# Performance work log

Measured on AMD Instinct MI355X. Metric: run time of the kernel, lower is better.

The kernel has to match this reference:

```python
import jax, jax.numpy as jnp
import numpy as np

B, C, H, L = 4, 1, 1024, 8192
KD, NS = 64, 4  # kernel_dim, num_scales


def _interp_linear(x, out_len):
    """F.interpolate(mode='linear', align_corners=False) along last axis."""
    in_len = x.shape[-1]
    if out_len == in_len:
        return x
    scale = out_len / in_len
    coord = (jnp.arange(out_len, dtype=jnp.float32) + 0.5) / scale - 0.5
    coord = jnp.clip(coord, 0.0, in_len - 1)
    lo = jnp.floor(coord).astype(jnp.int32)
    hi = jnp.minimum(lo + 1, in_len - 1)
    w = coord - lo.astype(jnp.float32)
    return x[..., lo] * (1.0 - w) + x[..., hi] * w


def setup_inputs() -> dict:
    key = jax.random.key(0)
    ks = jax.random.split(key, 8)
    u = jax.random.normal(ks[0], (B, H, L), jnp.float32)
    k0 = jax.random.normal(ks[1], (C, H, KD), jnp.float32)
    k1 = jax.random.normal(ks[2], (C, H, KD), jnp.float32)
    k2 = jax.random.normal(ks[3], (C, H, KD), jnp.float32)
    k3 = jax.random.normal(ks[4], (C, H, KD), jnp.float32)
    D = jax.random.normal(ks[5], (C, H), jnp.float32)
    W = jax.random.normal(ks[6], (H, C * H), jnp.float32) / np.float32(np.sqrt(C * H))
    b = jnp.zeros((H,), jnp.float32)
    return {"u": u, "k0": k0, "k1": k1, "k2": k2, "k3": k3, "D": D, "W": W, "b": b}


def reference(u, k0, k1, k2, k3, D, W, b):
    Lq = u.shape[-1]
    kernels = [k0, k1, k2, k3]
    total = KD * 2 ** (NS - 1)  # 512
    # multi-scale kernel build: interpolate -> right-pad -> scale -> sum
    parts = []
    for i in range(NS):
        ki = _interp_linear(kernels[i], KD * 2 ** i)
        ki = jnp.pad(ki, ((0, 0), (0, 0), (0, total - KD * 2 ** i)))
        parts.append(ki * (2.0 ** (NS - i - 1)))
    k = parts[0] + parts[1] + parts[2] + parts[3]  # (C,H,512)
    # fit to sequence length L
    if k.shape[-1] > Lq:
        k = k[..., :Lq]
    elif k.shape[-1] < Lq:
        k = jnp.pad(k, ((0, 0), (0, 0), (0, Lq - k.shape[-1])))
    # detached kernel norm
    knorm = jax.lax.stop_gradient(
        jnp.linalg.norm(k, axis=-1, keepdims=True))
    k = k / knorm
    # FFT long convolution
    n = 2 * Lq
    k_f = jnp.fft.rfft(k, n=n)              # (C,H,L+1) complex
    u_f = jnp.fft.rfft(u, n=n)              # (B,H,L+1) complex
    y_f = jnp.einsum('bhl,chl->bchl', u_f, k_f)
    y = jnp.fft.irfft(y_f, n=n)[..., :Lq]   # (B,C,H,L)
    # D skip (outer product)
    y = y + jnp.einsum('bhl,ch->bchl', u, D)
    y = y.reshape(y.shape[0], C * H, Lq)    # (B,C*H,L)
    # activation (exact gelu, torch default), dropout=Identity, norm=Identity
    y = jax.nn.gelu(y, approximate=False)
    # output_linear: 1x1 conv (C*H -> H) with bias, Identity post-activation
    y = jnp.einsum('bfl,of->bol', y, W) + b[None, :, None]
    return y
```

## Files before the change

kernel.cpp:

```cpp
#include <hip/hip_runtime.h>
#include <cstdint>
#include <cstddef>

#define HH 1024
#define LL 8192
#define NB 4
#define KD 64
#define KLEN 512

typedef float v4f  __attribute__((ext_vector_type(4)));
typedef float v16f __attribute__((ext_vector_type(16)));
typedef short v8s  __attribute__((ext_vector_type(8)));

__device__ __forceinline__ unsigned short f2bf(float f) {
  union { float f; unsigned int u; } x; x.f = f;
  unsigned int r = x.u + 0x7fffu + ((x.u >> 16) & 1u);
  return (unsigned short)(r >> 16);
}

__global__ __launch_bounds__(512) void build_k_kernel(
    const float* __restrict__ k0, const float* __restrict__ k1,
    const float* __restrict__ k2, const float* __restrict__ k3,
    float* __restrict__ kout) {
  __shared__ float lk[4][KD];
  __shared__ float red[512];
  const int h = blockIdx.x;
  const int t = threadIdx.x;
  if (t < 256) {
    int i = t >> 6, j = t & 63;
    const float* src = (i == 0) ? k0 : (i == 1) ? k1 : (i == 2) ? k2 : k3;
    lk[i][j] = src[h * KD + j];
  }
  __syncthreads();
  float kt = 0.f;
#pragma unroll
  for (int i = 0; i < 4; i++) {
    int len = KD << i;
    if (t < len) {
      float inv = 1.0f / (float)(1 << i);
      float c = ((float)t + 0.5f) * inv - 0.5f;
      c = fminf(fmaxf(c, 0.0f), 63.0f);
      int lo = (int)floorf(c);
      int hi = min(lo + 1, 63);
      float w = c - (float)lo;
      float v = lk[i][lo] * (1.0f - w) + lk[i][hi] * w;
      kt += v * (float)(1 << (3 - i));
    }
  }
  red[t] = kt * kt;
  __syncthreads();
  for (int s = 256; s > 0; s >>= 1) {
    if (t < s) red[t] += red[t + s];
    __syncthreads();
  }
  float norm = sqrtf(red[0]);
  kout[h * KLEN + t] = kt / norm;
}

__global__ void w2bf_kernel(const float* __restrict__ W,
                            unsigned short* __restrict__ Wb, int n) {
  int i = blockIdx.x * blockDim.x + threadIdx.x;
  if (i < n) Wb[i] = f2bf(W[i]);
}

__global__ __launch_bounds__(256) void conv_kernel(
    const float* __restrict__ u, const float* __restrict__ kk,
    const float* __restrict__ D, unsigned short* __restrict__ g) {
  __shared__ __align__(16) unsigned short Apk[34 * 512];
  __shared__ __align__(16) unsigned short su[512 + LL];
  __shared__ __align__(16) float skk[KLEN];

  const int h = blockIdx.x;
  const int tid = threadIdx.x;
  const int w = tid >> 6;
  const int ln = tid & 63;
  const int n = ln & 31;
  const int q = ln >> 5;

  if (tid < 128) *(float4*)(skk + tid * 4) = *(const float4*)(kk + (size_t)h * KLEN + tid * 4);
  __syncthreads();

#pragma unroll 4
  for (int e = 0; e < 68; ++e) {
    int idx = e * 256 + tid;
    int s = idx >> 9;
    int lane = (idx >> 3) & 63;
    int j = idx & 7;
    int m = lane & 31, q2 = lane >> 5;
    int c = ((s & 1) << 4) + (q2 << 3) + j;
    int t = ((s >> 1) << 5) + m - c;
    Apk[idx] = (t >= 0 && t < KLEN) ? f2bf(skk[t]) : (unsigned short)0;
  }

  const float Dh = D[h];
  const int b_base0 = 512 + 32 * (w * 64 + n) + 8 * q;
  const int b_base1 = b_base0 + 1024;

  for (int b = 0; b < NB; ++b) {
    __syncthreads();
    const float* __restrict__ urow = u + ((size_t)b * HH + h) * LL;
    if (tid < 64) {
      uint4 z; z.x = 0; z.y = 0; z.z = 0; z.w = 0;
      *(uint4*)(su + tid * 8) = z;
    }
#pragma unroll
    for (int r = 0; r < 8; ++r) {
      int i = r * 1024 + tid * 4;
      float4 v = *(const float4*)(urow + i);
      uint2 p;
      p.x = (unsigned)f2bf(v.x) | ((unsigned)f2bf(v.y) << 16);
      p.y = (unsigned)f2bf(v.z) | ((unsigned)f2bf(v.w) << 16);
      *(uint2*)(su + 512 + i) = p;
    }
    __syncthreads();

    v16f acc0, acc1;
#pragma unroll
    for (int r = 0; r < 16; ++r) { acc0[r] = 0.f; acc1[r] = 0.f; }

#pragma unroll
    for (int s = 0; s < 34; ++s) {
      const int off = ((s & 1) << 4) - ((s >> 1) << 5);
      v8s af = *(const v8s*)(Apk + (s << 9) + (ln << 3));
      v8s b0 = *(const v8s*)(su + b_base0 + off);
      v8s b1 = *(const v8s*)(su + b_base1 + off);
      acc0 = __builtin_amdgcn_mfma_f32_32x32x16_bf16(af, b0, acc0, 0, 0, 0);
      acc1 = __builtin_amdgcn_mfma_f32_32x32x16_bf16(af, b1, acc1, 0, 0, 0);
    }

    unsigned short* grow = g + ((size_t)b * HH + h) * LL;
#pragma unroll
    for (int t = 0; t < 2; ++t) {
      const int i0 = w * 64 + t * 32;
#pragma unroll
      for (int rg = 0; rg < 4; ++rg) {
        const int l = 32 * (i0 + n) + 8 * rg + 4 * q;
        float4 uu = *(const float4*)(urow + l);
        const float* up = (const float*)&uu;
        unsigned short hb[4];
#pragma unroll
        for (int rr = 0; rr < 4; ++rr) {
          float y = (t ? acc1[rg * 4 + rr] : acc0[rg * 4 + rr]) + Dh * up[rr];
          float ge = 0.5f * y * (1.0f + erff(y * 0.70710678118654752f));
          hb[rr] = f2bf(ge);
        }
        uint2 p;
        p.x = (unsigned)hb[0] | ((unsigned)hb[1] << 16);
        p.y = (unsigned)hb[2] | ((unsigned)hb[3] << 16);
        *(uint2*)(grow + l) = p;
      }
    }
  }
}

__global__ __launch_bounds__(256) void transpose_kernel(
    const unsigned short* __restrict__ g, unsigned short* __restrict__ gt) {
  __shared__ unsigned short s[64][65];
  const int bid = blockIdx.x;
  const int lc = bid & 127;
  const int hc = (bid >> 7) & 15;
  const int b = bid >> 11;
  const int l0 = lc * 64, h0 = hc * 64;
  const int tid = threadIdx.x;
  const int seg = tid & 7, rr = tid >> 3;
#pragma unroll
  for (int p = 0; p < 2; p++) {
    int r = p * 32 + rr;
    uint4 v = *(const uint4*)(g + (size_t)(b * HH + h0 + r) * LL + l0 + seg * 8);
    s[r][seg * 8 + 0] = (unsigned short)(v.x);
    s[r][seg * 8 + 1] = (unsigned short)(v.x >> 16);
    s[r][seg * 8 + 2] = (unsigned short)(v.y);
    s[r][seg * 8 + 3] = (unsigned short)(v.y >> 16);
    s[r][seg * 8 + 4] = (unsigned short)(v.z);
    s[r][seg * 8 + 5] = (unsigned short)(v.z >> 16);
    s[r][seg * 8 + 6] = (unsigned short)(v.w);
    s[r][seg * 8 + 7] = (unsigned short)(v.w >> 16);
  }
  __syncthreads();
#pragma unroll
  for (int p = 0; p < 2; p++) {
    int lr = p * 32 + rr;
    unsigned int a0 = (unsigned)s[seg * 8 + 0][lr] | ((unsigned)s[seg * 8 + 1][lr] << 16);
    unsigned int a1 = (unsigned)s[seg * 8 + 2][lr] | ((unsigned)s[seg * 8 + 3][lr] << 16);
    unsigned int a2 = (unsigned)s[seg * 8 + 4][lr] | ((unsigned)s[seg * 8 + 5][lr] << 16);
    unsigned int a3 = (unsigned)s[seg * 8 + 6][lr] | ((unsigned)s[seg * 8 + 7][lr] << 16);
    uint4 ov; ov.x = a0; ov.y = a1; ov.z = a2; ov.w = a3;
    *(uint4*)(gt + (size_t)(b * LL + l0 + lr) * HH + h0 + seg * 8) = ov;
  }
}

__device__ __forceinline__ void gll16(const void* g, void* l) {
  __builtin_amdgcn_global_load_lds(
      (const __attribute__((address_space(1))) unsigned int*)g,
      (__attribute__((address_space(3))) unsigned int*)l, 16, 0, 0);
}

__global__ __launch_bounds__(256) void gemm_kernel(
    const unsigned short* __restrict__ A,
    const unsigned short* __restrict__ Bt,
    const float* __restrict__ bias, float* __restrict__ out) {
  __shared__ __align__(16) unsigned short sA[128 * 32];
  __shared__ __align__(16) unsigned short sB[128 * 32];
  const int tid = threadIdx.x;
  const int wv = tid >> 6, ln = tid & 63;
  const int bid = blockIdx.x;
  const int mt = bid & 7, nt = bid >> 3;
  const int o0 = mt * 128, n0 = nt * 128;
  const int m16 = ln & 15, q4 = ln >> 4;
  const int wm = wv & 1, wn = wv >> 1;

  v4f acc[4][4];
#pragma unroll
  for (int i = 0; i < 4; i++)
#pragma unroll
    for (int j = 0; j < 4; j++) {
      v4f z = {0.f, 0.f, 0.f, 0.f};
      acc[i][j] = z;
    }

  const unsigned short* gptr[4];
  unsigned short* lptr[4];
#pragma unroll
  for (int qq = 0; qq < 4; qq++) {
    int c = wv * 4 + qq;
    int rr = (c & 7) * 16 + (ln >> 2);
    int cc = (ln & 3) * 8;
    if (c < 8) { gptr[qq] = A  + (size_t)(o0 + rr) * HH + cc; lptr[qq] = sA + c * 512; }
    else       { gptr[qq] = Bt + (size_t)(n0 + rr) * HH + cc; lptr[qq] = sB + (c - 8) * 512; }
  }

  for (int kk = 0; kk < 32; kk++) {
    const int k0 = kk * 32;
#pragma unroll
    for (int qq = 0; qq < 4; qq++) gll16(gptr[qq] + k0, lptr[qq]);
    __syncthreads();
    v8s af[4], bf4[4];
#pragma unroll
    for (int i = 0; i < 4; i++)
      af[i] = *(const v8s*)&sA[(wm * 64 + i * 16 + m16) * 32 + q4 * 8];
#pragma unroll
    for (int i = 0; i < 4; i++)
      bf4[i] = *(const v8s*)&sB[(wn * 64 + i * 16 + m16) * 32 + q4 * 8];
#pragma unroll
    for (int i = 0; i < 4; i++)
#pragma unroll
      for (int j = 0; j < 4; j++)
        acc[i][j] = __builtin_amdgcn_mfma_f32_16x16x32_bf16(af[i], bf4[j], acc[i][j], 0, 0, 0);
    __syncthreads();
  }

#pragma unroll
  for (int i = 0; i < 4; i++) {
    const int ob = o0 + wm * 64 + i * 16 + q4 * 4;
#pragma unroll
    for (int j = 0; j < 4; j++) {
      const int nn = n0 + wn * 64 + j * 16 + m16;
      const int bb = nn >> 13;
      const int l = nn & (LL - 1);
#pragma unroll
      for (int r = 0; r < 4; r++) {
        const int o = ob + r;
        out[(size_t)(bb * HH + o) * LL + l] = acc[i][j][r] + bias[o];
      }
    }
  }
}

extern "C" void kernel_launch(void* const* d_in, const int* in_sizes, int n_in,
                              void* d_out, int out_size, void* d_ws, size_t ws_size,
                              hipStream_t stream) {
  const float* u   = (const float*)d_in[0];
  const float* k0  = (const float*)d_in[1];
  const float* k1  = (const float*)d_in[2];
  const float* k2  = (const float*)d_in[3];
  const float* k3  = (const float*)d_in[4];
  const float* D   = (const float*)d_in[5];
  const float* W   = (const float*)d_in[6];
  const float* bia = (const float*)d_in[7];
  float* out = (float*)d_out;

  char* ws = (char*)d_ws;
  unsigned short* gt = (unsigned short*)ws;
  float* kws         = (float*)(ws + (size_t)67108864);
  unsigned short* Wb = (unsigned short*)(ws + (size_t)69206016);
  unsigned short* g = (unsigned short*)d_out;

  build_k_kernel<<<HH, 512, 0, stream>>>(k0, k1, k2, k3, kws);
  w2bf_kernel<<<(HH * HH + 255) / 256, 256, 0, stream>>>(W, Wb, HH * HH);
  conv_kernel<<<HH, 256, 0, stream>>>(u, kws, D, g);
  transpose_kernel<<<NB * 16 * 128, 256, 0, stream>>>(g, gt);
  gemm_kernel<<<8 * 256, 256, 0, stream>>>(Wb, gt, bia, out);
}
```

Baseline: 401.1 us.

## Split conv over batch halves, swizzle LDS input, reuse bf16 u for skip

The conv kernel now launches two blocks per channel, each covering two batches, so twice as many workgroups share the conv work. The shared-memory copy of u uses an XOR swizzle meant to cut bank conflicts on the MFMA B-operand loads. The D-skip term now reads bf16 u from LDS instead of reloading fp32 u from global memory. The trade-offs are that the Toeplitz A matrix is built twice per channel and the skip term loses precision from bf16 rounding.

```diff
diff --git a/kernel.cpp b/kernel.cpp
--- a/kernel.cpp
+++ b/kernel.cpp
@@ -16,6 +16,14 @@
   union { float f; unsigned int u; } x; x.f = f;
   unsigned int r = x.u + 0x7fffu + ((x.u >> 16) & 1u);
   return (unsigned short)(r >> 16);
+}
+__device__ __forceinline__ float bf2f(unsigned int s) {
+  union { unsigned int u; float f; } x; x.u = s << 16; return x.f;
+}
+
+__device__ __forceinline__ int swz(int L) {
+  int u = L >> 3;
+  return ((u ^ ((u >> 2) & 7)) << 3) | (L & 7);
 }
 
 __global__ __launch_bounds__(512) void build_k_kernel(
@@ -70,7 +78,8 @@
   __shared__ __align__(16) unsigned short su[512 + LL];
   __shared__ __align__(16) float skk[KLEN];
 
-  const int h = blockIdx.x;
+  const int h = blockIdx.x >> 1;
+  const int bp = (blockIdx.x & 1) * 2;
   const int tid = threadIdx.x;
   const int w = tid >> 6;
   const int ln = tid & 63;
@@ -93,15 +102,15 @@
   }
 
   const float Dh = D[h];
-  const int b_base0 = 512 + 32 * (w * 64 + n) + 8 * q;
-  const int b_base1 = b_base0 + 1024;
-
-  for (int b = 0; b < NB; ++b) {
+  const int XB = (w * 64 + n) << 5;
+
+  for (int bi = 0; bi < 2; ++bi) {
+    const int b = bp + bi;
     __syncthreads();
     const float* __restrict__ urow = u + ((size_t)b * HH + h) * LL;
-    if (tid < 64) {
-      uint4 z; z.x = 0; z.y = 0; z.z = 0; z.w = 0;
-      *(uint4*)(su + tid * 8) = z;
+    if (tid < 128) {
+      uint2 z; z.x = 0; z.y = 0;
+      *(uint2*)(su + swz(tid * 4)) = z;
     }
 #pragma unroll
     for (int r = 0; r < 8; ++r) {
@@ -110,7 +119,7 @@
       uint2 p;
       p.x = (unsigned)f2bf(v.x) | ((unsigned)f2bf(v.y) << 16);
       p.y = (unsigned)f2bf(v.z) | ((unsigned)f2bf(v.w) << 16);
-      *(uint2*)(su + 512 + i) = p;
+      *(uint2*)(su + swz(512 + i)) = p;
     }
     __syncthreads();
 
@@ -122,8 +131,9 @@
     for (int s = 0; s < 34; ++s) {
       const int off = ((s & 1) << 4) - ((s >> 1) << 5);
       v8s af = *(const v8s*)(Apk + (s << 9) + (ln << 3));
-      v8s b0 = *(const v8s*)(su + b_base0 + off);
-      v8s b1 = *(const v8s*)(su + b_base1 + off);
+      const int p0 = swz(512 + XB + (q << 3) + off);
+      v8s b0 = *(const v8s*)(su + p0);
+      v8s b1 = *(const v8s*)(su + p0 + 1024);
       acc0 = __builtin_amdgcn_mfma_f32_32x32x16_bf16(af, b0, acc0, 0, 0, 0);
       acc1 = __builtin_amdgcn_mfma_f32_32x32x16_bf16(af, b1, acc1, 0, 0, 0);
     }
@@ -135,8 +145,10 @@
 #pragma unroll
       for (int rg = 0; rg < 4; ++rg) {
         const int l = 32 * (i0 + n) + 8 * rg + 4 * q;
-        float4 uu = *(const float4*)(urow + l);
-        const float* up = (const float*)&uu;
+        uint2 uu = *(const uint2*)(su + swz(512 + l));
+        float up[4];
+        up[0] = bf2f(uu.x & 0xffffu); up[1] = bf2f(uu.x >> 16);
+        up[2] = bf2f(uu.y & 0xffffu); up[3] = bf2f(uu.y >> 16);
         unsigned short hb[4];
 #pragma unroll
         for (int rr = 0; rr < 4; ++rr) {
@@ -287,7 +299,7 @@
 
   build_k_kernel<<<HH, 512, 0, stream>>>(k0, k1, k2, k3, kws);
   w2bf_kernel<<<(HH * HH + 255) / 256, 256, 0, stream>>>(W, Wb, HH * HH);
-  conv_kernel<<<HH, 256, 0, stream>>>(u, kws, D, g);
+  conv_kernel<<<2 * HH, 256, 0, stream>>>(u, kws, D, g);
   transpose_kernel<<<NB * 16 * 128, 256, 0, stream>>>(g, gt);
   gemm_kernel<<<8 * 256, 256, 0, stream>>>(Wb, gt, bia, out);
 }
```

Result: no change. 404.0 us (+0.7%).
